# Kernel tuning notes

Measured on AMD Instinct MI355X. Metric: run time of the kernel, lower is better.

## Reference

```python
import jax, jax.numpy as jnp
import numpy as np

B, S, D = 1024, 256, 256  # batch, n_class, feature dim (g = n_component = 1)


def setup_inputs() -> dict:
    key = jax.random.key(0)
    k1, k2, k3 = jax.random.split(key, 3)
    x = jax.random.normal(k1, (B, D), dtype=jnp.float32)
    mu_p = jax.random.normal(k2, (S, 1, D), dtype=jnp.float32)
    sigma_p = jax.random.normal(k3, (S, 1, D, D), dtype=jnp.float32)
    return {"x": x, "mu_p": mu_p, "sigma_p": sigma_p}


def _log_probs(x, mu_p, sigma_p):
    sp = sigma_p[:, 0]            # (S, D, D), component index g=0
    mu = mu_p[:, 0]               # (S, D)
    # parameter_enforcing: m = sigma_p^T @ sigma_p (PSD);
    # mean of (real) eigenvalues of m == trace(m)/D, so the ridge term is
    # 0.01 * (trace(m)/D) * I, making sigma symmetric positive definite.
    m = jnp.einsum('skd,ske->sde', sp, sp)                      # (S, D, D)
    ridge = 0.01 * (jnp.trace(m, axis1=-2, axis2=-1) / D)       # (S,)
    sigma = m + ridge[:, None, None] * jnp.eye(D, dtype=m.dtype)
    # MVN log_prob via Cholesky: logdet = 2*sum(log diag L),
    # maha = || L^{-1} (x - mu) ||^2
    L = jnp.linalg.cholesky(sigma)                              # (S, D, D)
    logdet = 2.0 * jnp.sum(jnp.log(jnp.diagonal(L, axis1=-2, axis2=-1)), -1)  # (S,)
    diff = x[None, :, :] - mu[:, None, :]                       # (S, B, D)
    # batched triangular solve per class: y = L^{-1} diff^T -> (S, D, B)
    y = jax.vmap(lambda Ls, ds: jax.scipy.linalg.solve_triangular(Ls, ds.T, lower=True))(L, diff)
    maha = jnp.sum(y * y, axis=1)                               # (S, B)
    log2pi = jnp.log(2.0 * jnp.pi).astype(x.dtype)
    logp = -0.5 * (D * log2pi + logdet[:, None] + maha)         # (S, B)
    return logp.T                                               # (B, S)


def reference(x, mu_p, sigma_p):
    return _log_probs(x, mu_p, sigma_p)
```

## Files before the change

kernel.cpp:

```cpp
#include <hip/hip_runtime.h>
#include <math.h>


#define LOG2PI_D 470.4965290007924f

typedef __attribute__((ext_vector_type(8))) short bf16x8;
typedef __attribute__((ext_vector_type(4))) float f32x4;

__device__ __forceinline__ unsigned bf16rtn(float f) {
  unsigned u = __float_as_uint(f);
  return (u + 0x7FFFu + ((u >> 16) & 1u)) >> 16;
}
__device__ __forceinline__ unsigned packhl(float v) {
  unsigned h = bf16rtn(v);
  float hf = __uint_as_float(h << 16);
  unsigned l = bf16rtn(v - hf);
  return (h << 16) | l;
}

__global__ __launch_bounds__(256) void k_gram(const float* __restrict__ sp,
                                              float* __restrict__ L,
                                              float* __restrict__ ridge_out) {
  __shared__ unsigned Hb[4 * 128 * 20];
  unsigned* AH = Hb;
  unsigned* AL = Hb + 128 * 20;
  unsigned* BH = Hb + 2 * 128 * 20;
  unsigned* BL = Hb + 3 * 128 * 20;
  int p = blockIdx.y, s = blockIdx.x;
  int bi = (p ? 128 : 0), bj = (p == 2 ? 128 : 0);
  const float* A = sp + (size_t)s * 65536;
  float* C = L + (size_t)s * 65536;
  int tid = threadIdx.x, w = tid >> 6, lane = tid & 63;
  int q = lane >> 4, n = lane & 15;
  int mt_[2] = {w, 7 - w};
  f32x4 acc[2][8] = {};
  int c = tid & 127, g = tid >> 7;

  float va[16], vb[16];
#pragma unroll
  for (int u = 0; u < 16; ++u) {
    va[u] = A[(size_t)(g * 16 + u) * 256 + bi + c];
    if (p == 1) vb[u] = A[(size_t)(g * 16 + u) * 256 + bj + c];
  }

  for (int ks = 0; ks < 8; ++ks) {
    __syncthreads();
    {
      unsigned hw[8], lw[8];
#pragma unroll
      for (int m = 0; m < 8; ++m) {
        float v0 = va[2 * m], v1 = va[2 * m + 1];
        unsigned h0 = bf16rtn(v0), h1 = bf16rtn(v1);
        float r0 = v0 - __uint_as_float(h0 << 16);
        float r1 = v1 - __uint_as_float(h1 << 16);
        hw[m] = h0 | (h1 << 16);
        lw[m] = bf16rtn(r0) | (bf16rtn(r1) << 16);
      }
      *(uint4*)&AH[c * 20 + g * 8] = make_uint4(hw[0], hw[1], hw[2], hw[3]);
      *(uint4*)&AH[c * 20 + g * 8 + 4] = make_uint4(hw[4], hw[5], hw[6], hw[7]);
      *(uint4*)&AL[c * 20 + g * 8] = make_uint4(lw[0], lw[1], lw[2], lw[3]);
      *(uint4*)&AL[c * 20 + g * 8 + 4] = make_uint4(lw[4], lw[5], lw[6], lw[7]);
      if (p == 1) {
#pragma unroll
        for (int m = 0; m < 8; ++m) {
          float v0 = vb[2 * m], v1 = vb[2 * m + 1];
          unsigned h0 = bf16rtn(v0), h1 = bf16rtn(v1);
          float r0 = v0 - __uint_as_float(h0 << 16);
          float r1 = v1 - __uint_as_float(h1 << 16);
          hw[m] = h0 | (h1 << 16);
          lw[m] = bf16rtn(r0) | (bf16rtn(r1) << 16);
        }
        *(uint4*)&BH[c * 20 + g * 8] = make_uint4(hw[0], hw[1], hw[2], hw[3]);
        *(uint4*)&BH[c * 20 + g * 8 + 4] = make_uint4(hw[4], hw[5], hw[6], hw[7]);
        *(uint4*)&BL[c * 20 + g * 8] = make_uint4(lw[0], lw[1], lw[2], lw[3]);
        *(uint4*)&BL[c * 20 + g * 8 + 4] = make_uint4(lw[4], lw[5], lw[6], lw[7]);
      }
    }
    __syncthreads();
    if (ks < 7) {
      int r0g = (ks + 1) * 32 + g * 16;
#pragma unroll
      for (int u = 0; u < 16; ++u) {
        va[u] = A[(size_t)(r0g + u) * 256 + bi + c];
        if (p == 1) vb[u] = A[(size_t)(r0g + u) * 256 + bj + c];
      }
    }
    const unsigned* TBH = (p == 1) ? BH : AH;
    const unsigned* TBL = (p == 1) ? BL : AL;
    bf16x8 Ah[2], Al[2];
#pragma unroll
    for (int t = 0; t < 2; ++t) {
      int col = mt_[t] * 16 + n;
      Ah[t] = *(const bf16x8*)&AH[col * 20 + q * 4];
      Al[t] = *(const bf16x8*)&AL[col * 20 + q * 4];
    }
    int ntmax = (p == 1) ? 8 : (8 - w);
    for (int nt = 0; nt < ntmax; ++nt) {
      bf16x8 bh = *(const bf16x8*)&TBH[(nt * 16 + n) * 20 + q * 4];
      bf16x8 bl = *(const bf16x8*)&TBL[(nt * 16 + n) * 20 + q * 4];
#pragma unroll
      for (int t = 0; t < 2; ++t) {
        if (p == 1 || nt <= mt_[t]) {
          acc[t][nt] = __builtin_amdgcn_mfma_f32_16x16x32_bf16(Ah[t], bh, acc[t][nt], 0, 0, 0);
          acc[t][nt] = __builtin_amdgcn_mfma_f32_16x16x32_bf16(Ah[t], bl, acc[t][nt], 0, 0, 0);
          acc[t][nt] = __builtin_amdgcn_mfma_f32_16x16x32_bf16(Al[t], bh, acc[t][nt], 0, 0, 0);
        }
      }
    }
  }
  if (p != 1) {
    float dsum = 0.f;
#pragma unroll
    for (int t = 0; t < 2; ++t) {
      if ((n >> 2) == q) dsum += acc[t][mt_[t]][n & 3];
    }
    dsum += __shfl_down(dsum, 32, 64);
    dsum += __shfl_down(dsum, 16, 64);
    dsum += __shfl_down(dsum, 8, 64);
    dsum += __shfl_down(dsum, 4, 64);
    dsum += __shfl_down(dsum, 2, 64);
    dsum += __shfl_down(dsum, 1, 64);
    if (lane == 0) atomicAdd(&ridge_out[s], dsum * (0.01f / 256.0f));
  }
  float* slab = (float*)Hb;
  for (int t = 0; t < 2; ++t) {
    __syncthreads();
#pragma unroll
    for (int nt = 0; nt < 8; ++nt)
#pragma unroll
      for (int r = 0; r < 4; ++r)
        slab[w * 2048 + (q * 4 + r) * 128 + nt * 16 + n] = acc[t][nt][r];
    __syncthreads();
#pragma unroll
    for (int it = 0; it < 8; ++it) {
      int idx = tid + it * 256;
      int row = idx >> 5, c4 = idx & 31;
      int wsrc = row >> 4, r16 = row & 15;
      int rt = t ? (7 - wsrc) : wsrc;
      if (p == 1 || (c4 >> 2) <= rt) {
        int d = bi + rt * 16 + r16;
        *(float4*)(C + (size_t)d * 256 + bj + c4 * 4) =
            *(float4*)&slab[wsrc * 2048 + r16 * 128 + c4 * 4];
      }
    }
  }
}

__global__ __launch_bounds__(1024) void k_factor(float* __restrict__ L,
                                                 const float* __restrict__ ridge_buf) {
  extern __shared__ float lds[];
  float* P = lds;
  float* W = lds + 64 * 68;
  float* WT = lds + 2 * 64 * 68;
  float* T = lds + 3 * 64 * 68;
  int s = blockIdx.x;
  float* M = L + (size_t)s * 65536;
  int tid = threadIdx.x;
  int k4 = tid & 15, r64 = tid >> 4;
  float ridge = ridge_buf[s];

  for (int kb = 0; kb < 4; ++kb) {
    int base = kb * 64;
    __syncthreads();
    *(float4*)&P[r64 * 68 + k4 * 4] =
        *(const float4*)(M + (size_t)(base + r64) * 256 + base + k4 * 4);
    __syncthreads();
    if (tid < 64) P[tid * 68 + tid] += ridge;
    __syncthreads();
    {
      int eo = tid & 63, ro = tid >> 6;
      for (int cb = 0; cb < 16; ++cb) {
        int c0 = cb * 4;
        float g00 = P[c0 * 68 + c0];
        float g10 = P[(c0 + 1) * 68 + c0], g11 = P[(c0 + 1) * 68 + c0 + 1];
        float g20 = P[(c0 + 2) * 68 + c0], g21 = P[(c0 + 2) * 68 + c0 + 1],
              g22 = P[(c0 + 2) * 68 + c0 + 2];
        float g30 = P[(c0 + 3) * 68 + c0], g31 = P[(c0 + 3) * 68 + c0 + 1],
              g32 = P[(c0 + 3) * 68 + c0 + 2], g33 = P[(c0 + 3) * 68 + c0 + 3];
        float l00 = sqrtf(g00), r0 = 1.f / l00;
        float l10 = g10 * r0, l20 = g20 * r0, l30 = g30 * r0;
        float l11 = sqrtf(g11 - l10 * l10), r1 = 1.f / l11;
        float l21 = (g21 - l20 * l10) * r1, l31 = (g31 - l30 * l10) * r1;
        float l22 = sqrtf(g22 - l20 * l20 - l21 * l21), r2 = 1.f / l22;
        float l32 = (g32 - l30 * l20 - l31 * l21) * r2;
        float l33 = sqrtf(g33 - l30 * l30 - l31 * l31 - l32 * l32), r3 = 1.f / l33;
        int e = c0 + 4 + eo;
        if (e < 64) {
          float p0 = P[e * 68 + c0], p1 = P[e * 68 + c0 + 1];
          float p2 = P[e * 68 + c0 + 2], p3 = P[e * 68 + c0 + 3];
          float le0 = p0 * r0;
          float le1 = (p1 - le0 * l10) * r1;
          float le2 = (p2 - le0 * l20 - le1 * l21) * r2;
          float le3 = (p3 - le0 * l30 - le1 * l31 - le2 * l32) * r3;
          for (int r = c0 + 4 + ro; r < 64; r += 16) {
            float q0 = P[r * 68 + c0], q1 = P[r * 68 + c0 + 1];
            float q2 = P[r * 68 + c0 + 2], q3 = P[r * 68 + c0 + 3];
            float lr0 = q0 * r0;
            float lr1 = (q1 - lr0 * l10) * r1;
            float lr2 = (q2 - lr0 * l20 - lr1 * l21) * r2;
            float lr3 = (q3 - lr0 * l30 - lr1 * l31 - lr2 * l32) * r3;
            P[r * 68 + e] -= lr0 * le0 + lr1 * le1 + lr2 * le2 + lr3 * le3;
          }
        }
        __syncthreads();
      }
    }
    {
      int cb = tid >> 4, lane16 = tid & 15;
      int c0 = cb * 4;
      float vals[4][4];
      int rows[4], nr = 0;
      if (tid < 256) {
        float g00 = P[c0 * 68 + c0];
        float g10 = P[(c0 + 1) * 68 + c0], g11 = P[(c0 + 1) * 68 + c0 + 1];
        float g20 = P[(c0 + 2) * 68 + c0], g21 = P[(c0 + 2) * 68 + c0 + 1],
              g22 = P[(c0 + 2) * 68 + c0 + 2];
        float g30 = P[(c0 + 3) * 68 + c0], g31 = P[(c0 + 3) * 68 + c0 + 1],
              g32 = P[(c0 + 3) * 68 + c0 + 2], g33 = P[(c0 + 3) * 68 + c0 + 3];
        float l00 = sqrtf(g00), r0 = 1.f / l00;
        float l10 = g10 * r0, l20 = g20 * r0, l30 = g30 * r0;
        float l11 = sqrtf(g11 - l10 * l10), r1 = 1.f / l11;
        float l21 = (g21 - l20 * l10) * r1, l31 = (g31 - l30 * l10) * r1;
        float l22 = sqrtf(g22 - l20 * l20 - l21 * l21), r2 = 1.f / l22;
        float l32 = (g32 - l30 * l20 - l31 * l21) * r2;
        float l33 = sqrtf(g33 - l30 * l30 - l31 * l31 - l32 * l32), r3 = 1.f / l33;
        for (int r = c0 + lane16; r < 64; r += 16) {
          int i = r - c0;
          if (i == 0) { vals[nr][0] = l00; vals[nr][1] = 0; vals[nr][2] = 0; vals[nr][3] = 0; }
          else if (i == 1) { vals[nr][0] = l10; vals[nr][1] = l11; vals[nr][2] = 0; vals[nr][3] = 0; }
          else if (i == 2) { vals[nr][0] = l20; vals[nr][1] = l21; vals[nr][2] = l22; vals[nr][3] = 0; }
          else if (i == 3) { vals[nr][0] = l30; vals[nr][1] = l31; vals[nr][2] = l32; vals[nr][3] = l33; }
          else {
            float q0 = P[r * 68 + c0], q1 = P[r * 68 + c0 + 1];
            float q2 = P[r * 68 + c0 + 2], q3 = P[r * 68 + c0 + 3];
            float lr0 = q0 * r0;
            float lr1 = (q1 - lr0 * l10) * r1;
            float lr2 = (q2 - lr0 * l20 - lr1 * l21) * r2;
            float lr3 = (q3 - lr0 * l30 - lr1 * l31 - lr2 * l32) * r3;
            vals[nr][0] = lr0; vals[nr][1] = lr1; vals[nr][2] = lr2; vals[nr][3] = lr3;
          }
          rows[nr++] = r;
        }
      }
      __syncthreads();
      if (tid < 256) {
        for (int u = 0; u < nr; ++u) {
          int r = rows[u];
          P[r * 68 + c0] = vals[u][0];
          P[r * 68 + c0 + 1] = vals[u][1];
          P[r * 68 + c0 + 2] = vals[u][2];
          P[r * 68 + c0 + 3] = vals[u][3];
        }
      }
    }
    __syncthreads();
    for (int idx = tid; idx < 64 * 68; idx += 1024) W[idx] = 0.f;
    __syncthreads();
    for (int rb4 = 0; rb4 < 16; ++rb4) {
      int k0 = rb4 * 4;
      if (tid < 256) {
        int i = tid >> 6, cc = tid & 63;
        int row = k0 + i;
        float ssum = 0.f;
        for (int k = 0; k < k0; ++k) ssum += P[row * 68 + k] * W[k * 68 + cc];
        WT[i * 68 + cc] = ssum;
      }
      __syncthreads();
      if (tid < 64) {
        int cc = tid;
        float d00 = P[(k0 + 0) * 68 + k0];
        float d10 = P[(k0 + 1) * 68 + k0], d11 = P[(k0 + 1) * 68 + k0 + 1];
        float d20 = P[(k0 + 2) * 68 + k0], d21 = P[(k0 + 2) * 68 + k0 + 1],
              d22 = P[(k0 + 2) * 68 + k0 + 2];
        float d30 = P[(k0 + 3) * 68 + k0], d31 = P[(k0 + 3) * 68 + k0 + 1],
              d32 = P[(k0 + 3) * 68 + k0 + 2], d33 = P[(k0 + 3) * 68 + k0 + 3];
        float e0 = (cc == k0) ? 1.f : 0.f, e1 = (cc == k0 + 1) ? 1.f : 0.f;
        float e2 = (cc == k0 + 2) ? 1.f : 0.f, e3 = (cc == k0 + 3) ? 1.f : 0.f;
        float x0 = (e0 - WT[0 * 68 + cc]) / d00;
        float x1 = (e1 - WT[1 * 68 + cc] - d10 * x0) / d11;
        float x2 = (e2 - WT[2 * 68 + cc] - d20 * x0 - d21 * x1) / d22;
        float x3 = (e3 - WT[3 * 68 + cc] - d30 * x0 - d31 * x1 - d32 * x2) / d33;
        W[(k0 + 0) * 68 + cc] = x0;
        W[(k0 + 1) * 68 + cc] = x1;
        W[(k0 + 2) * 68 + cc] = x2;
        W[(k0 + 3) * 68 + cc] = x3;
      }
      __syncthreads();
    }
    {
      float4 v = *(float4*)&W[r64 * 68 + k4 * 4];
      WT[(k4 * 4 + 0) * 68 + r64] = v.x;
      WT[(k4 * 4 + 1) * 68 + r64] = v.y;
      WT[(k4 * 4 + 2) * 68 + r64] = v.z;
      WT[(k4 * 4 + 3) * 68 + r64] = v.w;
    }
    __syncthreads();
    *(float4*)(M + (size_t)(base + r64) * 256 + base + k4 * 4) = *(float4*)&W[r64 * 68 + k4 * 4];
    int nrt = 3 - kb;
    for (int rt0 = 0; rt0 < nrt; rt0 += 2) {
      int pr = tid >> 9, t2 = tid & 511;
      int my = rt0 + pr;
      bool act = my < nrt;
      float* Tb = pr ? T : P;
      int k42 = t2 & 15, rbl = t2 >> 4;
      int ty2 = t2 >> 4, tx2 = t2 & 15;
      int g0 = base + 64 + my * 64;
      __syncthreads();
      if (act) {
#pragma unroll
        for (int r = rbl; r < 64; r += 32) {
          float4 v = *(const float4*)(M + (size_t)(g0 + r) * 256 + base + k42 * 4);
          Tb[(k42 * 4 + 0) * 68 + r] = v.x;
          Tb[(k42 * 4 + 1) * 68 + r] = v.y;
          Tb[(k42 * 4 + 2) * 68 + r] = v.z;
          Tb[(k42 * 4 + 3) * 68 + r] = v.w;
        }
      }
      __syncthreads();
      float acc[2][4] = {};
      if (act) {
        for (int k = 0; k < 64; ++k) {
          float a0 = Tb[k * 68 + ty2 * 2], a1 = Tb[k * 68 + ty2 * 2 + 1];
          float b[4];
          *(float4*)b = *(float4*)&WT[k * 68 + tx2 * 4];
#pragma unroll
          for (int j = 0; j < 4; ++j) {
            acc[0][j] += a0 * b[j];
            acc[1][j] += a1 * b[j];
          }
        }
      }
      __syncthreads();
      if (act) {
#pragma unroll
        for (int i = 0; i < 2; ++i)
          *(float4*)(M + (size_t)(g0 + ty2 * 2 + i) * 256 + base + tx2 * 4) =
              make_float4(acc[i][0], acc[i][1], acc[i][2], acc[i][3]);
#pragma unroll
        for (int i = 0; i < 2; ++i)
#pragma unroll
          for (int j = 0; j < 4; ++j) Tb[(tx2 * 4 + j) * 68 + ty2 * 2 + i] = acc[i][j];
      }
      __syncthreads();
      if (act) {
#pragma unroll
        for (int r = rbl; r < 64; r += 32)
          *(float4*)(M + (size_t)(base + r) * 256 + g0 + k42 * 4) = *(float4*)&Tb[r * 68 + k42 * 4];
      }
    }
    int np = ((3 - kb) * (4 - kb)) / 2;
    for (int p0 = 0; p0 < np; p0 += 2) {
      int pr = tid >> 9, t2 = tid & 511;
      int my = p0 + pr;
      bool act = my < np;
      int ti = 1, tj = 1;
      {
        int cnt = 0;
        for (int a = kb + 1; a < 4; ++a)
          for (int b = kb + 1; b <= a; ++b) {
            if (cnt == my) { ti = a; tj = b; }
            ++cnt;
          }
      }
      float* Pi = pr ? WT : P;
      float* Pj = pr ? T : W;
      int k42 = t2 & 15, rbl = t2 >> 4;
      int ty2 = t2 >> 4, tx2 = t2 & 15;
      __syncthreads();
      float acc[2][4];
      if (act) {
#pragma unroll
        for (int k = rbl; k < 64; k += 32) {
          *(float4*)&Pi[k * 68 + k42 * 4] =
              *(const float4*)(M + (size_t)(base + k) * 256 + ti * 64 + k42 * 4);
          *(float4*)&Pj[k * 68 + k42 * 4] =
              *(const float4*)(M + (size_t)(base + k) * 256 + tj * 64 + k42 * 4);
        }
#pragma unroll
        for (int i = 0; i < 2; ++i)
          *(float4*)&acc[i][0] =
              *(const float4*)(M + (size_t)(ti * 64 + ty2 * 2 + i) * 256 + tj * 64 + tx2 * 4);
      }
      __syncthreads();
      if (act) {
        for (int k = 0; k < 64; ++k) {
          float a0 = Pi[k * 68 + ty2 * 2], a1 = Pi[k * 68 + ty2 * 2 + 1];
          float b[4];
          *(float4*)b = *(float4*)&Pj[k * 68 + tx2 * 4];
#pragma unroll
          for (int j = 0; j < 4; ++j) {
            acc[0][j] -= a0 * b[j];
            acc[1][j] -= a1 * b[j];
          }
        }
#pragma unroll
        for (int i = 0; i < 2; ++i)
          *(float4*)(M + (size_t)(ti * 64 + ty2 * 2 + i) * 256 + tj * 64 + tx2 * 4) =
              make_float4(acc[i][0], acc[i][1], acc[i][2], acc[i][3]);
      }
    }
  }
}

__global__ __launch_bounds__(256) void k_invcol(float* __restrict__ Lw) {
  extern __shared__ float lds[];
  float* Bcol = lds;
  float* LW = lds + 3 * 64 * 68;
  float* Cs = LW + 64 * 68;
  int j = blockIdx.y, s = blockIdx.x;
  float* M = Lw + (size_t)s * 65536;
  unsigned* M32 = (unsigned*)M;
  int tid = threadIdx.x, k4 = tid & 15, rb = tid >> 4;
  int ty = tid >> 4, tx = tid & 15;

  for (int r = rb; r < 64; r += 16)
    *(float4*)&Bcol[r * 68 + k4 * 4] =
        *(const float4*)(M + (size_t)(j * 64 + r) * 256 + j * 64 + k4 * 4);
  __syncthreads();

  for (int i = j + 1; i < 4; ++i) {
    float acc[4][4] = {};
    for (int kk = j; kk < i; ++kk) {
      __syncthreads();
      for (int k = rb; k < 64; k += 16)
        *(float4*)&LW[k * 68 + k4 * 4] =
            *(const float4*)(M + (size_t)(kk * 64 + k) * 256 + i * 64 + k4 * 4);
      __syncthreads();
      float* Bk = Bcol + (kk - j) * 64 * 68;
#pragma unroll 4
      for (int k = 0; k < 64; ++k) {
        float a[4], b[4];
        *(float4*)a = *(float4*)&LW[k * 68 + ty * 4];
        *(float4*)b = *(float4*)&Bk[k * 68 + tx * 4];
#pragma unroll
        for (int r = 0; r < 4; ++r)
#pragma unroll
          for (int c = 0; c < 4; ++c) acc[r][c] += a[r] * b[c];
      }
    }
    __syncthreads();
#pragma unroll
    for (int r = 0; r < 4; ++r)
      *(float4*)&Cs[(ty * 4 + r) * 68 + tx * 4] =
          make_float4(acc[r][0], acc[r][1], acc[r][2], acc[r][3]);
    for (int r = rb; r < 64; r += 16) {
      float4 v = *(const float4*)(M + (size_t)(i * 64 + r) * 256 + i * 64 + k4 * 4);
      LW[(k4 * 4 + 0) * 68 + r] = v.x;
      LW[(k4 * 4 + 1) * 68 + r] = v.y;
      LW[(k4 * 4 + 2) * 68 + r] = v.z;
      LW[(k4 * 4 + 3) * 68 + r] = v.w;
    }
    __syncthreads();
    float d[4][4] = {};
#pragma unroll 4
    for (int k = 0; k < 64; ++k) {
      float a[4], b[4];
      *(float4*)a = *(float4*)&LW[k * 68 + ty * 4];
      *(float4*)b = *(float4*)&Cs[k * 68 + tx * 4];
#pragma unroll
      for (int r = 0; r < 4; ++r)
#pragma unroll
        for (int c = 0; c < 4; ++c) d[r][c] -= a[r] * b[c];
    }
    float* Bi = Bcol + (i - j) * 64 * 68;
#pragma unroll
    for (int r = 0; r < 4; ++r) {
      if (i < 3)
        *(float4*)&Bi[(ty * 4 + r) * 68 + tx * 4] =
            make_float4(d[r][0], d[r][1], d[r][2], d[r][3]);
      uint4 pu;
      pu.x = packhl(d[r][0]); pu.y = packhl(d[r][1]);
      pu.z = packhl(d[r][2]); pu.w = packhl(d[r][3]);
      *(uint4*)(M32 + (size_t)(i * 64 + ty * 4 + r) * 256 + j * 64 + tx * 4) = pu;
    }
    __syncthreads();
  }
}

__global__ __launch_bounds__(512) void k_maha(const float* __restrict__ x,
                                              const float* __restrict__ mu_p,
                                              const float* __restrict__ Lw,
                                              float* __restrict__ out) {
  __shared__ __align__(16) short Bh[128 * 40];
  __shared__ __align__(16) short Bl[128 * 40];
  __shared__ float Red[1025];
  int s = blockIdx.x, b0 = blockIdx.y * 128;
  const float* Mf = Lw + (size_t)s * 65536;
  const unsigned* M32 = (const unsigned*)Mf;
  int tid = threadIdx.x, w = tid >> 6, lane = tid & 63;
  int q = lane >> 4, n = lane & 15;
  int mt_[2] = {w, 15 - w};
  f32x4 acc[2][8] = {};

  for (int ks = 0; ks < 8; ++ks) {
    __syncthreads();
    {
      int b = tid >> 2, q8 = tid & 3;
      const float* xp = x + (size_t)(b0 + b) * 256 + ks * 32 + q8 * 8;
      const float* mp = mu_p + (size_t)s * 256 + ks * 32 + q8 * 8;
      float4 xa = ((const float4*)xp)[0], xb = ((const float4*)xp)[1];
      float4 ma = ((const float4*)mp)[0], mb = ((const float4*)mp)[1];
      float dv[8] = {xa.x - ma.x, xa.y - ma.y, xa.z - ma.z, xa.w - ma.w,
                     xb.x - mb.x, xb.y - mb.y, xb.z - mb.z, xb.w - mb.w};
      unsigned h[8], l[8];
#pragma unroll
      for (int jj = 0; jj < 8; ++jj) {
        h[jj] = bf16rtn(dv[jj]);
        float hf = __uint_as_float(h[jj] << 16);
        l[jj] = bf16rtn(dv[jj] - hf);
      }
      *(uint4*)&Bh[b * 40 + q8 * 8] =
          make_uint4(h[0] | (h[1] << 16), h[2] | (h[3] << 16),
                     h[4] | (h[5] << 16), h[6] | (h[7] << 16));
      *(uint4*)&Bl[b * 40 + q8 * 8] =
          make_uint4(l[0] | (l[1] << 16), l[2] | (l[3] << 16),
                     l[4] | (l[5] << 16), l[6] | (l[7] << 16));
    }
    __syncthreads();
    bf16x8 Ah[2], Al[2];
    bool act[2];
#pragma unroll
    for (int t = 0; t < 2; ++t) {
      int mt = mt_[t];
      act[t] = ks < ((mt + 2) >> 1);
      if (act[t]) {
        const unsigned* ap = M32 + (size_t)(mt * 16 + n) * 256 + ks * 32 + q * 8;
        uint4 u0 = *(const uint4*)ap;
        uint4 u1 = *(const uint4*)(ap + 4);
        unsigned uu[8] = {u0.x, u0.y, u0.z, u0.w, u1.x, u1.y, u1.z, u1.w};
        if ((ks >> 1) == (mt >> 2)) {
#pragma unroll
          for (int jj = 0; jj < 8; ++jj) {
            float f = __uint_as_float(uu[jj]);
            unsigned hh = bf16rtn(f);
            float hf = __uint_as_float(hh << 16);
            Ah[t][jj] = (short)hh;
            Al[t][jj] = (short)bf16rtn(f - hf);
          }
        } else {
#pragma unroll
          for (int jj = 0; jj < 8; ++jj) {
            Ah[t][jj] = (short)(uu[jj] >> 16);
            Al[t][jj] = (short)(uu[jj] & 0xffffu);
          }
        }
      }
    }
#pragma unroll
    for (int bsub = 0; bsub < 8; ++bsub) {
      bf16x8 bh = *(const bf16x8*)&Bh[(bsub * 16 + n) * 40 + q * 8];
      bf16x8 bl = *(const bf16x8*)&Bl[(bsub * 16 + n) * 40 + q * 8];
#pragma unroll
      for (int t = 0; t < 2; ++t) {
        if (act[t]) {
          acc[t][bsub] = __builtin_amdgcn_mfma_f32_16x16x32_bf16(Ah[t], bh, acc[t][bsub], 0, 0, 0);
          acc[t][bsub] = __builtin_amdgcn_mfma_f32_16x16x32_bf16(Ah[t], bl, acc[t][bsub], 0, 0, 0);
          acc[t][bsub] = __builtin_amdgcn_mfma_f32_16x16x32_bf16(Al[t], bh, acc[t][bsub], 0, 0, 0);
        }
      }
    }
  }
#pragma unroll
  for (int bsub = 0; bsub < 8; ++bsub) {
    float v = 0.f;
#pragma unroll
    for (int t = 0; t < 2; ++t)
#pragma unroll
      for (int r = 0; r < 4; ++r) v += acc[t][bsub][r] * acc[t][bsub][r];
    v += __shfl_xor(v, 16, 64);
    v += __shfl_xor(v, 32, 64);
    if (lane < 16) Red[w * 128 + bsub * 16 + lane] = v;
  }
  if (w == 0) {
    float ld = 0.f;
#pragma unroll
    for (int c = 0; c < 4; ++c)
      ld += logf(Mf[(size_t)(c * 64 + lane) * 256 + c * 64 + lane]);
    ld += __shfl_down(ld, 32, 64);
    ld += __shfl_down(ld, 16, 64);
    ld += __shfl_down(ld, 8, 64);
    ld += __shfl_down(ld, 4, 64);
    ld += __shfl_down(ld, 2, 64);
    ld += __shfl_down(ld, 1, 64);
    if (lane == 0) Red[1024] = ld;
  }
  __syncthreads();
  if (tid < 128) {
    float mh = 0.f;
#pragma unroll
    for (int w2 = 0; w2 < 8; ++w2) mh += Red[w2 * 128 + tid];
    out[(size_t)(b0 + tid) * 256 + s] = -0.5f * (LOG2PI_D - 2.0f * Red[1024] + mh);
  }
}

extern "C" void kernel_launch(void* const* d_in, const int* in_sizes, int n_in,
                              void* d_out, int out_size, void* d_ws, size_t ws_size,
                              hipStream_t stream) {
  const float* x = (const float*)d_in[0];
  const float* mu = (const float*)d_in[1];
  const float* sp = (const float*)d_in[2];
  float* out = (float*)d_out;
  float* L = (float*)d_ws;

  const int fact_lds = 4 * 64 * 68 * 4;
  const int invc_lds = 5 * 64 * 68 * 4;
  (void)hipFuncSetAttribute((const void*)k_factor,
                            hipFuncAttributeMaxDynamicSharedMemorySize, fact_lds);
  (void)hipFuncSetAttribute((const void*)k_invcol,
                            hipFuncAttributeMaxDynamicSharedMemorySize, invc_lds);

  k_gram<<<dim3(256, 3), 256, 0, stream>>>(sp, L, out);
  k_factor<<<256, 1024, fact_lds, stream>>>(L, out);
  k_invcol<<<dim3(256, 3), 256, invc_lds, stream>>>(L);
  k_maha<<<dim3(256, 8), 512, 0, stream>>>(x, mu, L, out);
}
```

Measured before the change: 645.7 us.

## Fuse triangular inverse into factor kernel and keep panels resident in LDS

Merges the separate k_invcol kernel into k_factor so that the blocked L inverse columns are computed by the same workgroup after factorization. Trailing-update panels are kept in LDS across the loop, so the next diagonal block is written straight to LDS instead of going through global memory and being reloaded. The diagonal-block inverse solve now takes 8 rows per step instead of 4, which halves the number of barriers. The trade-offs are that only 256 of 1024 threads do the inverse GEMMs, parallelism drops from 768 to 256 blocks for that phase, and LDS use grows to six panels.

```diff
diff --git a/kernel.cpp b/kernel.cpp
--- a/kernel.cpp
+++ b/kernel.cpp
@@ -3,6 +3,8 @@
 
 
 #define LOG2PI_D 470.4965290007924f
+#define PS 68
+#define PANEL (64*68)
 
 typedef __attribute__((ext_vector_type(8))) short bf16x8;
 typedef __attribute__((ext_vector_type(4))) float f32x4;
@@ -150,11 +152,11 @@
                                                  const float* __restrict__ ridge_buf) {
   extern __shared__ float lds[];
   float* P = lds;
-  float* W = lds + 64 * 68;
-  float* WT = lds + 2 * 64 * 68;
-  float* T = lds + 3 * 64 * 68;
+  float* W = lds + PANEL;
+  float* WT = lds + 2 * PANEL;
   int s = blockIdx.x;
   float* M = L + (size_t)s * 65536;
+  unsigned* M32 = (unsigned*)M;
   int tid = threadIdx.x;
   int k4 = tid & 15, r64 = tid >> 4;
   float ridge = ridge_buf[s];
@@ -162,21 +164,22 @@
   for (int kb = 0; kb < 4; ++kb) {
     int base = kb * 64;
     __syncthreads();
-    *(float4*)&P[r64 * 68 + k4 * 4] =
-        *(const float4*)(M + (size_t)(base + r64) * 256 + base + k4 * 4);
-    __syncthreads();
-    if (tid < 64) P[tid * 68 + tid] += ridge;
+    if (kb == 0)
+      *(float4*)&P[r64 * PS + k4 * 4] =
+          *(const float4*)(M + (size_t)(base + r64) * 256 + base + k4 * 4);
+    __syncthreads();
+    if (tid < 64) P[tid * PS + tid] += ridge;
     __syncthreads();
     {
       int eo = tid & 63, ro = tid >> 6;
       for (int cb = 0; cb < 16; ++cb) {
         int c0 = cb * 4;
-        float g00 = P[c0 * 68 + c0];
-        float g10 = P[(c0 + 1) * 68 + c0], g11 = P[(c0 + 1) * 68 + c0 + 1];
-        float g20 = P[(c0 + 2) * 68 + c0], g21 = P[(c0 + 2) * 68 + c0 + 1],
-              g22 = P[(c0 + 2) * 68 + c0 + 2];
-        float g30 = P[(c0 + 3) * 68 + c0], g31 = P[(c0 + 3) * 68 + c0 + 1],
-              g32 = P[(c0 + 3) * 68 + c0 + 2], g33 = P[(c0 + 3) * 68 + c0 + 3];
+        float g00 = P[c0 * PS + c0];
+        float g10 = P[(c0 + 1) * PS + c0], g11 = P[(c0 + 1) * PS + c0 + 1];
+        float g20 = P[(c0 + 2) * PS + c0], g21 = P[(c0 + 2) * PS + c0 + 1],
+              g22 = P[(c0 + 2) * PS + c0 + 2];
+        float g30 = P[(c0 + 3) * PS + c0], g31 = P[(c0 + 3) * PS + c0 + 1],
+              g32 = P[(c0 + 3) * PS + c0 + 2], g33 = P[(c0 + 3) * PS + c0 + 3];
         float l00 = sqrtf(g00), r0 = 1.f / l00;
         float l10 = g10 * r0, l20 = g20 * r0, l30 = g30 * r0;
         float l11 = sqrtf(g11 - l10 * l10), r1 = 1.f / l11;
@@ -186,20 +189,20 @@
         float l33 = sqrtf(g33 - l30 * l30 - l31 * l31 - l32 * l32), r3 = 1.f / l33;
         int e = c0 + 4 + eo;
         if (e < 64) {
-          float p0 = P[e * 68 + c0], p1 = P[e * 68 + c0 + 1];
-          float p2 = P[e * 68 + c0 + 2], p3 = P[e * 68 + c0 + 3];
+          float p0 = P[e * PS + c0], p1 = P[e * PS + c0 + 1];
+          float p2 = P[e * PS + c0 + 2], p3 = P[e * PS + c0 + 3];
           float le0 = p0 * r0;
           float le1 = (p1 - le0 * l10) * r1;
           float le2 = (p2 - le0 * l20 - le1 * l21) * r2;
           float le3 = (p3 - le0 * l30 - le1 * l31 - le2 * l32) * r3;
           for (int r = c0 + 4 + ro; r < 64; r += 16) {
-            float q0 = P[r * 68 + c0], q1 = P[r * 68 + c0 + 1];
-            float q2 = P[r * 68 + c0 + 2], q3 = P[r * 68 + c0 + 3];
+            float q0 = P[r * PS + c0], q1 = P[r * PS + c0 + 1];
+            float q2 = P[r * PS + c0 + 2], q3 = P[r * PS + c0 + 3];
             float lr0 = q0 * r0;
             float lr1 = (q1 - lr0 * l10) * r1;
             float lr2 = (q2 - lr0 * l20 - lr1 * l21) * r2;
             float lr3 = (q3 - lr0 * l30 - lr1 * l31 - lr2 * l32) * r3;
-            P[r * 68 + e] -= lr0 * le0 + lr1 * le1 + lr2 * le2 + lr3 * le3;
+            P[r * PS + e] -= lr0 * le0 + lr1 * le1 + lr2 * le2 + lr3 * le3;
           }
         }
         __syncthreads();
@@ -211,12 +214,12 @@
       float vals[4][4];
       int rows[4], nr = 0;
       if (tid < 256) {
-        float g00 = P[c0 * 68 + c0];
-        float g10 = P[(c0 + 1) * 68 + c0], g11 = P[(c0 + 1) * 68 + c0 + 1];
-        float g20 = P[(c0 + 2) * 68 + c0], g21 = P[(c0 + 2) * 68 + c0 + 1],
-              g22 = P[(c0 + 2) * 68 + c0 + 2];
-        float g30 = P[(c0 + 3) * 68 + c0], g31 = P[(c0 + 3) * 68 + c0 + 1],
-              g32 = P[(c0 + 3) * 68 + c0 + 2], g33 = P[(c0 + 3) * 68 + c0 + 3];
+        float g00 = P[c0 * PS + c0];
+        float g10 = P[(c0 + 1) * PS + c0], g11 = P[(c0 + 1) * PS + c0 + 1];
+        float g20 = P[(c0 + 2) * PS + c0], g21 = P[(c0 + 2) * PS + c0 + 1],
+              g22 = P[(c0 + 2) * PS + c0 + 2];
+        float g30 = P[(c0 + 3) * PS + c0], g31 = P[(c0 + 3) * PS + c0 + 1],
+              g32 = P[(c0 + 3) * PS + c0 + 2], g33 = P[(c0 + 3) * PS + c0 + 3];
         float l00 = sqrtf(g00), r0 = 1.f / l00;
         float l10 = g10 * r0, l20 = g20 * r0, l30 = g30 * r0;
         float l11 = sqrtf(g11 - l10 * l10), r1 = 1.f / l11;
@@ -231,8 +234,8 @@
           else if (i == 2) { vals[nr][0] = l20; vals[nr][1] = l21; vals[nr][2] = l22; vals[nr][3] = 0; }
           else if (i == 3) { vals[nr][0] = l30; vals[nr][1] = l31; vals[nr][2] = l32; vals[nr][3] = l33; }
           else {
-            float q0 = P[r * 68 + c0], q1 = P[r * 68 + c0 + 1];
-            float q2 = P[r * 68 + c0 + 2], q3 = P[r * 68 + c0 + 3];
+            float q0 = P[r * PS + c0], q1 = P[r * PS + c0 + 1];
+            float q2 = P[r * PS + c0 + 2], q3 = P[r * PS + c0 + 3];
             float lr0 = q0 * r0;
             float lr1 = (q1 - lr0 * l10) * r1;
             float lr2 = (q2 - lr0 * l20 - lr1 * l21) * r2;
@@ -246,62 +249,56 @@
       if (tid < 256) {
         for (int u = 0; u < nr; ++u) {
           int r = rows[u];
-          P[r * 68 + c0] = vals[u][0];
-          P[r * 68 + c0 + 1] = vals[u][1];
-          P[r * 68 + c0 + 2] = vals[u][2];
-          P[r * 68 + c0 + 3] = vals[u][3];
-        }
-      }
-    }
-    __syncthreads();
-    for (int idx = tid; idx < 64 * 68; idx += 1024) W[idx] = 0.f;
-    __syncthreads();
-    for (int rb4 = 0; rb4 < 16; ++rb4) {
-      int k0 = rb4 * 4;
-      if (tid < 256) {
+          P[r * PS + c0] = vals[u][0];
+          P[r * PS + c0 + 1] = vals[u][1];
+          P[r * PS + c0 + 2] = vals[u][2];
+          P[r * PS + c0 + 3] = vals[u][3];
+        }
+      }
+    }
+    __syncthreads();
+    for (int idx = tid; idx < PANEL; idx += 1024) W[idx] = 0.f;
+    __syncthreads();
+    for (int r8 = 0; r8 < 8; ++r8) {
+      int k0 = r8 * 8;
+      if (tid < 512) {
         int i = tid >> 6, cc = tid & 63;
         int row = k0 + i;
-        float ssum = 0.f;
-        for (int k = 0; k < k0; ++k) ssum += P[row * 68 + k] * W[k * 68 + cc];
-        WT[i * 68 + cc] = ssum;
+        float ss = 0.f;
+        for (int k = 0; k < k0; ++k) ss += P[row * PS + k] * W[k * PS + cc];
+        WT[i * PS + cc] = ss;
       }
       __syncthreads();
       if (tid < 64) {
         int cc = tid;
-        float d00 = P[(k0 + 0) * 68 + k0];
-        float d10 = P[(k0 + 1) * 68 + k0], d11 = P[(k0 + 1) * 68 + k0 + 1];
-        float d20 = P[(k0 + 2) * 68 + k0], d21 = P[(k0 + 2) * 68 + k0 + 1],
-              d22 = P[(k0 + 2) * 68 + k0 + 2];
-        float d30 = P[(k0 + 3) * 68 + k0], d31 = P[(k0 + 3) * 68 + k0 + 1],
-              d32 = P[(k0 + 3) * 68 + k0 + 2], d33 = P[(k0 + 3) * 68 + k0 + 3];
-        float e0 = (cc == k0) ? 1.f : 0.f, e1 = (cc == k0 + 1) ? 1.f : 0.f;
-        float e2 = (cc == k0 + 2) ? 1.f : 0.f, e3 = (cc == k0 + 3) ? 1.f : 0.f;
-        float x0 = (e0 - WT[0 * 68 + cc]) / d00;
-        float x1 = (e1 - WT[1 * 68 + cc] - d10 * x0) / d11;
-        float x2 = (e2 - WT[2 * 68 + cc] - d20 * x0 - d21 * x1) / d22;
-        float x3 = (e3 - WT[3 * 68 + cc] - d30 * x0 - d31 * x1 - d32 * x2) / d33;
-        W[(k0 + 0) * 68 + cc] = x0;
-        W[(k0 + 1) * 68 + cc] = x1;
-        W[(k0 + 2) * 68 + cc] = x2;
-        W[(k0 + 3) * 68 + cc] = x3;
+        float x[8];
+#pragma unroll
+        for (int m = 0; m < 8; ++m) {
+          float v = ((cc == k0 + m) ? 1.f : 0.f) - WT[m * PS + cc];
+#pragma unroll
+          for (int u = 0; u < 8; ++u)
+            if (u < m) v -= P[(k0 + m) * PS + k0 + u] * x[u];
+          x[m] = v / P[(k0 + m) * PS + k0 + m];
+          W[(k0 + m) * PS + cc] = x[m];
+        }
       }
       __syncthreads();
     }
     {
-      float4 v = *(float4*)&W[r64 * 68 + k4 * 4];
-      WT[(k4 * 4 + 0) * 68 + r64] = v.x;
-      WT[(k4 * 4 + 1) * 68 + r64] = v.y;
-      WT[(k4 * 4 + 2) * 68 + r64] = v.z;
-      WT[(k4 * 4 + 3) * 68 + r64] = v.w;
-    }
-    __syncthreads();
-    *(float4*)(M + (size_t)(base + r64) * 256 + base + k4 * 4) = *(float4*)&W[r64 * 68 + k4 * 4];
+      float4 v = *(float4*)&W[r64 * PS + k4 * 4];
+      WT[(k4 * 4 + 0) * PS + r64] = v.x;
+      WT[(k4 * 4 + 1) * PS + r64] = v.y;
+      WT[(k4 * 4 + 2) * PS + r64] = v.z;
+      WT[(k4 * 4 + 3) * PS + r64] = v.w;
+    }
+    __syncthreads();
+    *(float4*)(M + (size_t)(base + r64) * 256 + base + k4 * 4) = *(float4*)&W[r64 * PS + k4 * 4];
     int nrt = 3 - kb;
     for (int rt0 = 0; rt0 < nrt; rt0 += 2) {
       int pr = tid >> 9, t2 = tid & 511;
       int my = rt0 + pr;
       bool act = my < nrt;
-      float* Tb = pr ? T : P;
+      float* Tb = lds + (size_t)(3 + (act ? my : 0)) * PANEL;
       int k42 = t2 & 15, rbl = t2 >> 4;
       int ty2 = t2 >> 4, tx2 = t2 & 15;
       int g0 = base + 64 + my * 64;
@@ -310,19 +307,19 @@
 #pragma unroll
         for (int r = rbl; r < 64; r += 32) {
           float4 v = *(const float4*)(M + (size_t)(g0 + r) * 256 + base + k42 * 4);
-          Tb[(k42 * 4 + 0) * 68 + r] = v.x;
-          Tb[(k42 * 4 + 1) * 68 + r] = v.y;
-          Tb[(k42 * 4 + 2) * 68 + r] = v.z;
-          Tb[(k42 * 4 + 3) * 68 + r] = v.w;
+          Tb[(k42 * 4 + 0) * PS + r] = v.x;
+          Tb[(k42 * 4 + 1) * PS + r] = v.y;
+          Tb[(k42 * 4 + 2) * PS + r] = v.z;
+          Tb[(k42 * 4 + 3) * PS + r] = v.w;
         }
       }
       __syncthreads();
       float acc[2][4] = {};
       if (act) {
         for (int k = 0; k < 64; ++k) {
-          float a0 = Tb[k * 68 + ty2 * 2], a1 = Tb[k * 68 + ty2 * 2 + 1];
+          float a0 = Tb[k * PS + ty2 * 2], a1 = Tb[k * PS + ty2 * 2 + 1];
           float b[4];
-          *(float4*)b = *(float4*)&WT[k * 68 + tx2 * 4];
+          *(float4*)b = *(float4*)&WT[k * PS + tx2 * 4];
 #pragma unroll
           for (int j = 0; j < 4; ++j) {
             acc[0][j] += a0 * b[j];
@@ -334,26 +331,23 @@
       if (act) {
 #pragma unroll
         for (int i = 0; i < 2; ++i)
-          *(float4*)(M + (size_t)(g0 + ty2 * 2 + i) * 256 + base + tx2 * 4) =
-              make_float4(acc[i][0], acc[i][1], acc[i][2], acc[i][3]);
-#pragma unroll
-        for (int i = 0; i < 2; ++i)
-#pragma unroll
-          for (int j = 0; j < 4; ++j) Tb[(tx2 * 4 + j) * 68 + ty2 * 2 + i] = acc[i][j];
+#pragma unroll
+          for (int j = 0; j < 4; ++j) Tb[(tx2 * 4 + j) * PS + ty2 * 2 + i] = acc[i][j];
       }
       __syncthreads();
       if (act) {
 #pragma unroll
         for (int r = rbl; r < 64; r += 32)
-          *(float4*)(M + (size_t)(base + r) * 256 + g0 + k42 * 4) = *(float4*)&Tb[r * 68 + k42 * 4];
-      }
-    }
+          *(float4*)(M + (size_t)(base + r) * 256 + g0 + k42 * 4) = *(float4*)&Tb[r * PS + k42 * 4];
+      }
+    }
+    __syncthreads();
     int np = ((3 - kb) * (4 - kb)) / 2;
     for (int p0 = 0; p0 < np; p0 += 2) {
       int pr = tid >> 9, t2 = tid & 511;
       int my = p0 + pr;
       bool act = my < np;
-      int ti = 1, tj = 1;
+      int ti = kb + 1, tj = kb + 1;
       {
         int cnt = 0;
         for (int a = kb + 1; a < 4; ++a)
@@ -362,118 +356,117 @@
             ++cnt;
           }
       }
-      float* Pi = pr ? WT : P;
-      float* Pj = pr ? T : W;
-      int k42 = t2 & 15, rbl = t2 >> 4;
+      float* Pi = lds + (size_t)(3 + (ti - kb - 1)) * PANEL;
+      float* Pj = lds + (size_t)(3 + (tj - kb - 1)) * PANEL;
       int ty2 = t2 >> 4, tx2 = t2 & 15;
-      __syncthreads();
       float acc[2][4];
       if (act) {
-#pragma unroll
-        for (int k = rbl; k < 64; k += 32) {
-          *(float4*)&Pi[k * 68 + k42 * 4] =
-              *(const float4*)(M + (size_t)(base + k) * 256 + ti * 64 + k42 * 4);
-          *(float4*)&Pj[k * 68 + k42 * 4] =
-              *(const float4*)(M + (size_t)(base + k) * 256 + tj * 64 + k42 * 4);
-        }
 #pragma unroll
         for (int i = 0; i < 2; ++i)
           *(float4*)&acc[i][0] =
               *(const float4*)(M + (size_t)(ti * 64 + ty2 * 2 + i) * 256 + tj * 64 + tx2 * 4);
-      }
-      __syncthreads();
-      if (act) {
         for (int k = 0; k < 64; ++k) {
-          float a0 = Pi[k * 68 + ty2 * 2], a1 = Pi[k * 68 + ty2 * 2 + 1];
+          float a0 = Pi[k * PS + ty2 * 2], a1 = Pi[k * PS + ty2 * 2 + 1];
           float b[4];
-          *(float4*)b = *(float4*)&Pj[k * 68 + tx2 * 4];
+          *(float4*)b = *(float4*)&Pj[k * PS + tx2 * 4];
 #pragma unroll
           for (int j = 0; j < 4; ++j) {
             acc[0][j] -= a0 * b[j];
             acc[1][j] -= a1 * b[j];
           }
         }
-#pragma unroll
-        for (int i = 0; i < 2; ++i)
-          *(float4*)(M + (size_t)(ti * 64 + ty2 * 2 + i) * 256 + tj * 64 + tx2 * 4) =
-              make_float4(acc[i][0], acc[i][1], acc[i][2], acc[i][3]);
-      }
-    }
-  }
-}
-
-__global__ __launch_bounds__(256) void k_invcol(float* __restrict__ Lw) {
-  extern __shared__ float lds[];
-  float* Bcol = lds;
-  float* LW = lds + 3 * 64 * 68;
-  float* Cs = LW + 64 * 68;
-  int j = blockIdx.y, s = blockIdx.x;
-  float* M = Lw + (size_t)s * 65536;
-  unsigned* M32 = (unsigned*)M;
-  int tid = threadIdx.x, k4 = tid & 15, rb = tid >> 4;
-  int ty = tid >> 4, tx = tid & 15;
-
-  for (int r = rb; r < 64; r += 16)
-    *(float4*)&Bcol[r * 68 + k4 * 4] =
-        *(const float4*)(M + (size_t)(j * 64 + r) * 256 + j * 64 + k4 * 4);
-  __syncthreads();
-
-  for (int i = j + 1; i < 4; ++i) {
-    float acc[4][4] = {};
-    for (int kk = j; kk < i; ++kk) {
-      __syncthreads();
-      for (int k = rb; k < 64; k += 16)
-        *(float4*)&LW[k * 68 + k4 * 4] =
-            *(const float4*)(M + (size_t)(kk * 64 + k) * 256 + i * 64 + k4 * 4);
-      __syncthreads();
-      float* Bk = Bcol + (kk - j) * 64 * 68;
+        if (ti == tj && ti == kb + 1) {
+#pragma unroll
+          for (int i = 0; i < 2; ++i)
+            *(float4*)&P[(ty2 * 2 + i) * PS + tx2 * 4] =
+                make_float4(acc[i][0], acc[i][1], acc[i][2], acc[i][3]);
+        } else {
+#pragma unroll
+          for (int i = 0; i < 2; ++i)
+            *(float4*)(M + (size_t)(ti * 64 + ty2 * 2 + i) * 256 + tj * 64 + tx2 * 4) =
+                make_float4(acc[i][0], acc[i][1], acc[i][2], acc[i][3]);
+        }
+      }
+    }
+  }
+
+  {
+    float* Bcol = lds;
+    float* LW = lds + 3 * PANEL;
+    float* Cs = lds + 4 * PANEL;
+    int rb = tid >> 4;
+    int ty = tid >> 4, tx = tid & 15;
+    for (int j = 0; j < 3; ++j) {
+      __syncthreads();
+      for (int r = rb; r < 64; r += 16)
+        *(float4*)&Bcol[r * PS + k4 * 4] =
+            *(const float4*)(M + (size_t)(j * 64 + r) * 256 + j * 64 + k4 * 4);
+      __syncthreads();
+
+      for (int i = j + 1; i < 4; ++i) {
+        float acc[4][4] = {};
+        for (int kk = j; kk < i; ++kk) {
+          __syncthreads();
+          for (int k = rb; k < 64; k += 16)
+            *(float4*)&LW[k * PS + k4 * 4] =
+                *(const float4*)(M + (size_t)(kk * 64 + k) * 256 + i * 64 + k4 * 4);
+          __syncthreads();
+          float* Bk = Bcol + (kk - j) * PANEL;
+          if (tid < 256) {
 #pragma unroll 4
-      for (int k = 0; k < 64; ++k) {
-        float a[4], b[4];
-        *(float4*)a = *(float4*)&LW[k * 68 + ty * 4];
-        *(float4*)b = *(float4*)&Bk[k * 68 + tx * 4];
-#pragma unroll
-        for (int r = 0; r < 4; ++r)
-#pragma unroll
-          for (int c = 0; c < 4; ++c) acc[r][c] += a[r] * b[c];
-      }
-    }
-    __syncthreads();
-#pragma unroll
-    for (int r = 0; r < 4; ++r)
-      *(float4*)&Cs[(ty * 4 + r) * 68 + tx * 4] =
-          make_float4(acc[r][0], acc[r][1], acc[r][2], acc[r][3]);
-    for (int r = rb; r < 64; r += 16) {
-      float4 v = *(const float4*)(M + (size_t)(i * 64 + r) * 256 + i * 64 + k4 * 4);
-      LW[(k4 * 4 + 0) * 68 + r] = v.x;
-      LW[(k4 * 4 + 1) * 68 + r] = v.y;
-      LW[(k4 * 4 + 2) * 68 + r] = v.z;
-      LW[(k4 * 4 + 3) * 68 + r] = v.w;
-    }
-    __syncthreads();
-    float d[4][4] = {};
+            for (int k = 0; k < 64; ++k) {
+              float a[4], b[4];
+              *(float4*)a = *(float4*)&LW[k * PS + ty * 4];
+              *(float4*)b = *(float4*)&Bk[k * PS + tx * 4];
+#pragma unroll
+              for (int r = 0; r < 4; ++r)
+#pragma unroll
+                for (int cc = 0; cc < 4; ++cc) acc[r][cc] += a[r] * b[cc];
+            }
+          }
+        }
+        __syncthreads();
+        if (tid < 256) {
+#pragma unroll
+          for (int r = 0; r < 4; ++r)
+            *(float4*)&Cs[(ty * 4 + r) * PS + tx * 4] =
+                make_float4(acc[r][0], acc[r][1], acc[r][2], acc[r][3]);
+        }
+        for (int r = rb; r < 64; r += 16) {
+          float4 v = *(const float4*)(M + (size_t)(i * 64 + r) * 256 + i * 64 + k4 * 4);
+          LW[(k4 * 4 + 0) * PS + r] = v.x;
+          LW[(k4 * 4 + 1) * PS + r] = v.y;
+          LW[(k4 * 4 + 2) * PS + r] = v.z;
+          LW[(k4 * 4 + 3) * PS + r] = v.w;
+        }
+        __syncthreads();
+        if (tid < 256) {
+          float d[4][4] = {};
 #pragma unroll 4
-    for (int k = 0; k < 64; ++k) {
-      float a[4], b[4];
-      *(float4*)a = *(float4*)&LW[k * 68 + ty * 4];
-      *(float4*)b = *(float4*)&Cs[k * 68 + tx * 4];
-#pragma unroll
-      for (int r = 0; r < 4; ++r)
-#pragma unroll
-        for (int c = 0; c < 4; ++c) d[r][c] -= a[r] * b[c];
-    }
-    float* Bi = Bcol + (i - j) * 64 * 68;
-#pragma unroll
-    for (int r = 0; r < 4; ++r) {
-      if (i < 3)
-        *(float4*)&Bi[(ty * 4 + r) * 68 + tx * 4] =
-            make_float4(d[r][0], d[r][1], d[r][2], d[r][3]);
-      uint4 pu;
-      pu.x = packhl(d[r][0]); pu.y = packhl(d[r][1]);
-      pu.z = packhl(d[r][2]); pu.w = packhl(d[r][3]);
-      *(uint4*)(M32 + (size_t)(i * 64 + ty * 4 + r) * 256 + j * 64 + tx * 4) = pu;
-    }
-    __syncthreads();
+          for (int k = 0; k < 64; ++k) {
+            float a[4], b[4];
+            *(float4*)a = *(float4*)&LW[k * PS + ty * 4];
+            *(float4*)b = *(float4*)&Cs[k * PS + tx * 4];
+#pragma unroll
+            for (int r = 0; r < 4; ++r)
+#pragma unroll
+              for (int cc = 0; cc < 4; ++cc) d[r][cc] -= a[r] * b[cc];
+          }
+          float* Bi = Bcol + (i - j) * PANEL;
+#pragma unroll
+          for (int r = 0; r < 4; ++r) {
+            if (i < 3)
+              *(float4*)&Bi[(ty * 4 + r) * PS + tx * 4] =
+                  make_float4(d[r][0], d[r][1], d[r][2], d[r][3]);
+            uint4 pu;
+            pu.x = packhl(d[r][0]); pu.y = packhl(d[r][1]);
+            pu.z = packhl(d[r][2]); pu.w = packhl(d[r][3]);
+            *(uint4*)(M32 + (size_t)(i * 64 + ty * 4 + r) * 256 + j * 64 + tx * 4) = pu;
+          }
+        }
+        __syncthreads();
+      }
+    }
   }
 }
 
@@ -602,15 +595,11 @@
   float* out = (float*)d_out;
   float* L = (float*)d_ws;
 
-  const int fact_lds = 4 * 64 * 68 * 4;
-  const int invc_lds = 5 * 64 * 68 * 4;
+  const int fact_lds = 6 * PANEL * 4;
   (void)hipFuncSetAttribute((const void*)k_factor,
                             hipFuncAttributeMaxDynamicSharedMemorySize, fact_lds);
-  (void)hipFuncSetAttribute((const void*)k_invcol,
-                            hipFuncAttributeMaxDynamicSharedMemorySize, invc_lds);
 
   k_gram<<<dim3(256, 3), 256, 0, stream>>>(sp, L, out);
   k_factor<<<256, 1024, fact_lds, stream>>>(L, out);
-  k_invcol<<<dim3(256, 3), 256, invc_lds, stream>>>(L);
   k_maha<<<dim3(256, 8), 512, 0, stream>>>(x, mu, L, out);
 }
```

Result: faster. 569.6 us (-11.8%).
